# Kernel tuning notes

Hardware: AMD Instinct MI355X
Metric: run time of the kernel (lower is better)

The kernel has to match this reference:

```python
import jax, jax.numpy as jnp
import numpy as np

# Block-sparse linear config: W is (OUT_F, IN_F) in BSR form with BS x BS blocks,
OUT_F, IN_F, BS, K = 4096, 4096, 64, 32
NROW, NCOL = OUT_F // BS, IN_F // BS   # 64, 64
NNZB = NROW * K                         # 2048 nonzero blocks
BATCH = 8192


def setup_inputs() -> dict:
    key = jax.random.key(0)
    k1, k2, k3 = jax.random.split(key, 3)
    x = jax.random.normal(k1, (BATCH, IN_F), jnp.float32)
    values = jax.random.normal(k2, (NNZB, BS, BS), jnp.float32) * 0.02
    bias = jax.random.normal(k3, (OUT_F,), jnp.float32) * 0.01
    # BSR structure: K sorted, distinct column-block indices per block-row.
    cols = np.stack([np.sort((r + 2 * np.arange(K)) % NCOL) for r in range(NROW)])
    col_indices = jnp.asarray(cols.reshape(-1), jnp.int32)          # [NNZB]
    crow_indices = jnp.arange(NROW + 1, dtype=jnp.int32) * K        # [NROW+1]
    return {"x": x, "values": values, "bias": bias,
            "crow_indices": crow_indices, "col_indices": col_indices}


def reference(x, values, bias, crow_indices, col_indices):
    # Expand BSR row pointers to per-block row ids (structure is static/int).
    counts = jnp.diff(crow_indices)
    row_ids = jnp.repeat(jnp.arange(NROW), counts, total_repeat_length=NNZB)
    # Scatter nonzero blocks into a dense weight (only ~67 MB, cheap vs the GEMM).
    Wb = jnp.zeros((NROW, NCOL, BS, BS), values.dtype).at[row_ids, col_indices].set(values)
    W = Wb.transpose(0, 2, 1, 3).reshape(OUT_F, IN_F)  # [out_features, in_features]
    # forward: (W @ x.T).T + bias  ==  x @ W.T + bias
    return x @ W.T + bias
```

## Files before the change

kernel.cpp:

```cpp
#include <hip/hip_runtime.h>
#include <stdint.h>


#define BATCH   8192
#define IN_F    4096
#define OUT_F   4096
#define BS      64
#define NROW    64
#define NNZB    2048
#define BM      256
#define LDS_A_BYTES 32768
#define LDS_B_BYTES 16384
#define BUF_BYTES   (LDS_A_BYTES + LDS_B_BYTES)
#define NBUF    2

typedef float f32x4 __attribute__((ext_vector_type(4)));
typedef short s16x8 __attribute__((ext_vector_type(8)));

__device__ __forceinline__ void async_copy16(const void* g, void* l) {
  __builtin_amdgcn_global_load_lds(
      (__attribute__((address_space(1))) void*)g,
      (__attribute__((address_space(3))) void*)l, 16, 0, 0);
}

__device__ __forceinline__ unsigned short f32_to_bf16(float f) {
  union { float f; uint32_t u; } v; v.f = f;
  return (unsigned short)((v.u + 0x7FFFu + ((v.u >> 16) & 1u)) >> 16);
}

__global__ void cvt_kernel(const float4* __restrict__ xin,
                           const float4* __restrict__ win,
                           ushort4* __restrict__ xout,
                           ushort4* __restrict__ wout, int nx4, int ntot4) {
  int i = blockIdx.x * blockDim.x + threadIdx.x;
  if (i >= ntot4) return;
  const float4* src; ushort4* dst; int j;
  if (i < nx4) { src = xin; dst = xout; j = i; }
  else         { src = win; dst = wout; j = i - nx4; }
  float4 v = src[j];
  ushort4 o;
  o.x = f32_to_bf16(v.x); o.y = f32_to_bf16(v.y);
  o.z = f32_to_bf16(v.z); o.w = f32_to_bf16(v.w);
  dst[j] = o;
}

__global__ __launch_bounds__(512) void bsr_gemm_pair_kernel(
    const unsigned short* __restrict__ xb,
    const unsigned short* __restrict__ wb,
    const float* __restrict__ bias,
    const int* __restrict__ crow,
    const int* __restrict__ cols,
    float* __restrict__ out) {
  __shared__ alignas(16) char smem[NBUF * BUF_BYTES];

  const int tid = threadIdx.x;
  const int w   = tid >> 6;
  const int l   = tid & 63;
  const int wm  = w & 3;
  const int wn  = w >> 2;
  const int p   = blockIdx.x;
  const int rA  = ((p >> 1) << 2) + (p & 1);
  const int rB  = rA + 2;
  const int m0  = blockIdx.y * BM;

  const int startA = crow[rA], endA = crow[rA + 1];
  const int startB = crow[rB], endB = crow[rB + 1];

  const int lr = l & 15;
  const int q  = l >> 4;

  int cvA = (startA + l < endA) ? cols[startA + l] : 0;
  int cvB = (startB + l < endB) ? cols[startB + l] : 0;

  int myc = 0, mypk = 0;
  int nt = 0;
  {
    int ia = startA, ib = startB;
    const int clA = (endA > startA) ? endA - 1 : 0;
    const int clB = (endB > startB) ? endB - 1 : 0;
    while ((ia < endA) || (ib < endB)) {
      const int ca = (ia < endA) ? __shfl(cvA, ia - startA) : 0x7fffffff;
      const int cb = (ib < endB) ? __shfl(cvB, ib - startB) : 0x7fffffff;
      const int c  = min(ca, cb);
      const int hA = (ca == c);
      const int hB = (cb == c);
      const int sA = hA ? ia : clA;
      const int sB = hB ? ib : clB;
      if (nt == l) { myc = c; mypk = sA | (sB << 12) | (hA << 24) | (hB << 25); }
      ia += hA; ib += hB; ++nt;
    }
  }

  f32x4 acc[4][4];
#pragma unroll
  for (int mi = 0; mi < 4; ++mi)
#pragma unroll
    for (int ni = 0; ni < 4; ++ni) {
      f32x4 z = {0.f, 0.f, 0.f, 0.f};
      acc[mi][ni] = z;
    }

  const int srow = tid >> 3;
  const int sswz = ((tid & 7) ^ (srow & 7)) << 3;
  const unsigned short* agbase =
      xb + (size_t)(m0 + srow) * IN_F + sswz;
  const int bgoff = (srow << 6) + sswz;

  auto stage = [&](int t, int buf) {
    const int c  = __shfl(myc, t);
    const int pk = __shfl(mypk, t);
    const int sA = pk & 0xfff;
    const int sB = (pk >> 12) & 0xfff;
    char* const al = smem + buf * BUF_BYTES + tid * 16;
    char* const bl = smem + buf * BUF_BYTES + LDS_A_BYTES + tid * 16;
    const unsigned short* ag = agbase + (size_t)c * BS;
#pragma unroll
    for (int it = 0; it < 4; ++it)
      async_copy16(ag + (size_t)(it * 64) * IN_F, al + it * 8192);
    async_copy16(wb + ((size_t)sA << 12) + bgoff, bl);
    async_copy16(wb + ((size_t)sB << 12) + bgoff, bl + 8192);
  };

  if (nt > 0) stage(0, 0);
  __syncthreads();
  int cur = 0;
  for (int t = 0; t < nt; ++t) {
    if (t + 1 < nt) stage(t + 1, cur ^ 1);

    const int pk = __shfl(mypk, t);
    const char* const cbase = smem + cur * BUF_BYTES;
    if ((pk >> (24 + wn)) & 1) {
      __builtin_amdgcn_s_setprio(1);
#pragma unroll
      for (int ks = 0; ks < 2; ++ks) {
        const int chunk = (((ks << 2) + q) ^ (l & 7)) << 4;
        s16x8 af[4], bf[4];
#pragma unroll
        for (int mi = 0; mi < 4; ++mi)
          af[mi] = *(const s16x8*)(cbase +
                     ((wm << 6) + (mi << 4) + lr) * 128 + chunk);
#pragma unroll
        for (int ni = 0; ni < 4; ++ni)
          bf[ni] = *(const s16x8*)(cbase + LDS_A_BYTES + (wn << 13) +
                     ((ni << 4) + lr) * 128 + chunk);
#pragma unroll
        for (int mi = 0; mi < 4; ++mi)
#pragma unroll
          for (int ni = 0; ni < 4; ++ni)
            acc[mi][ni] = __builtin_amdgcn_mfma_f32_16x16x32_bf16(
                af[mi], bf[ni], acc[mi][ni], 0, 0, 0);
      }
      __builtin_amdgcn_s_setprio(0);
    }
    __syncthreads();
    cur ^= 1;
  }

  const int rW = wn ? rB : rA;
  const int colg = (rW << 6) + lr;
#pragma unroll
  for (int ni = 0; ni < 4; ++ni) {
    const float bv = bias[colg + (ni << 4)];
#pragma unroll
    for (int mi = 0; mi < 4; ++mi) {
      float* op = out +
          (size_t)(m0 + (wm << 6) + (mi << 4) + (q << 2)) * OUT_F +
          colg + (ni << 4);
#pragma unroll
      for (int e = 0; e < 4; ++e)
        op[(size_t)e * OUT_F] = acc[mi][ni][e] + bv;
    }
  }
}

__global__ void fallback_kernel(const float* __restrict__ x,
                                const float* __restrict__ vals,
                                const float* __restrict__ bias,
                                const int* __restrict__ crow,
                                const int* __restrict__ cols,
                                float* __restrict__ out) {
  int idx = blockIdx.x * 256 + threadIdx.x;
  int m = idx >> 12;
  int n = idx & 4095;
  int r = n >> 6, nl = n & 63;
  float s = 0.f;
  int e = crow[r + 1];
  for (int i = crow[r]; i < e; ++i) {
    const float* xp = x + (size_t)m * IN_F + cols[i] * 64;
    const float* wp = vals + ((size_t)i << 12) + nl * 64;
    for (int k = 0; k < 64; ++k) s += xp[k] * wp[k];
  }
  out[idx] = s + bias[n];
}

extern "C" void kernel_launch(void* const* d_in, const int* in_sizes, int n_in,
                              void* d_out, int out_size, void* d_ws,
                              size_t ws_size, hipStream_t stream) {
  const float* x    = (const float*)d_in[0];
  const float* vals = (const float*)d_in[1];
  const float* bias = (const float*)d_in[2];
  const int*   crow = (const int*)d_in[3];
  const int*   cols = (const int*)d_in[4];
  float* out = (float*)d_out;

  const size_t x_elems = (size_t)BATCH * IN_F;
  const size_t w_elems = (size_t)NNZB * BS * BS;
  const size_t need = (x_elems + w_elems) * 2;

  if (ws_size >= need) {
    unsigned short* xb = (unsigned short*)d_ws;
    unsigned short* wbp = xb + x_elems;
    const int nx4 = (int)(x_elems / 4);
    const int ntot4 = (int)((x_elems + w_elems) / 4);
    cvt_kernel<<<(ntot4 + 255) / 256, 256, 0, stream>>>(
        (const float4*)x, (const float4*)vals,
        (ushort4*)xb, (ushort4*)wbp, nx4, ntot4);
    dim3 grid(NROW / 2, BATCH / BM);
    bsr_gemm_pair_kernel<<<grid, 512, 0, stream>>>(xb, wbp, bias, crow, cols,
                                                   out);
  } else {
    fallback_kernel<<<(BATCH * OUT_F) / 256, 256, 0, stream>>>(
        x, vals, bias, crow, cols, out);
  }
}
```

Measured before the change: 418.5 us.

## Halve block to 256 threads with single LDS buffer and two blocks per CU

Shrinks the workgroup from 8 to 4 waves, so each wave computes a 128x64 tile (8x4 MFMA accumulators instead of 4x4). Double buffering is replaced by a single 48 KB LDS buffer, with barriers before and after each stage, and launch bounds request two blocks per CU. The aim is to get overlap from having several resident blocks rather than from in-block prefetch, and to raise MFMA work per LDS fragment load. The cost is that load latency is now exposed inside each block, and the larger accumulator set raises register pressure.

Measured after the change: 378.0 us. 1.11x faster.

```diff
diff --git a/kernel.cpp b/kernel.cpp
--- a/kernel.cpp
+++ b/kernel.cpp
@@ -9,10 +9,8 @@
 #define NROW    64
 #define NNZB    2048
 #define BM      256
-#define LDS_A_BYTES 32768
-#define LDS_B_BYTES 16384
-#define BUF_BYTES   (LDS_A_BYTES + LDS_B_BYTES)
-#define NBUF    2
+#define LDS_A_BYTES (BM * BS * 2)
+#define LDS_B_BYTES (2 * BS * BS * 2)
 
 typedef float f32x4 __attribute__((ext_vector_type(4)));
 typedef short s16x8 __attribute__((ext_vector_type(8)));
@@ -44,20 +42,20 @@
   dst[j] = o;
 }
 
-__global__ __launch_bounds__(512) void bsr_gemm_pair_kernel(
+__global__ __launch_bounds__(256, 2) void bsr_gemm_pair_kernel(
     const unsigned short* __restrict__ xb,
     const unsigned short* __restrict__ wb,
     const float* __restrict__ bias,
     const int* __restrict__ crow,
     const int* __restrict__ cols,
     float* __restrict__ out) {
-  __shared__ alignas(16) char smem[NBUF * BUF_BYTES];
+  __shared__ alignas(16) char smem[LDS_A_BYTES + LDS_B_BYTES];
 
   const int tid = threadIdx.x;
   const int w   = tid >> 6;
   const int l   = tid & 63;
-  const int wm  = w & 3;
-  const int wn  = w >> 2;
+  const int wm  = w & 1;
+  const int wn  = w >> 1;
   const int p   = blockIdx.x;
   const int rA  = ((p >> 1) << 2) + (p & 1);
   const int rB  = rA + 2;
@@ -91,9 +89,9 @@
     }
   }
 
-  f32x4 acc[4][4];
-#pragma unroll
-  for (int mi = 0; mi < 4; ++mi)
+  f32x4 acc[8][4];
+#pragma unroll
+  for (int mi = 0; mi < 8; ++mi)
 #pragma unroll
     for (int ni = 0; ni < 4; ++ni) {
       f32x4 z = {0.f, 0.f, 0.f, 0.f};
@@ -105,46 +103,48 @@
   const unsigned short* agbase =
       xb + (size_t)(m0 + srow) * IN_F + sswz;
   const int bgoff = (srow << 6) + sswz;
-
-  auto stage = [&](int t, int buf) {
+  char* const alds = smem + tid * 16;
+  char* const blds = smem + LDS_A_BYTES + tid * 16;
+
+  auto stage = [&](int t) {
+    const int pk = __shfl(mypk, t);
     const int c  = __shfl(myc, t);
-    const int pk = __shfl(mypk, t);
     const int sA = pk & 0xfff;
     const int sB = (pk >> 12) & 0xfff;
-    char* const al = smem + buf * BUF_BYTES + tid * 16;
-    char* const bl = smem + buf * BUF_BYTES + LDS_A_BYTES + tid * 16;
     const unsigned short* ag = agbase + (size_t)c * BS;
 #pragma unroll
-    for (int it = 0; it < 4; ++it)
-      async_copy16(ag + (size_t)(it * 64) * IN_F, al + it * 8192);
-    async_copy16(wb + ((size_t)sA << 12) + bgoff, bl);
-    async_copy16(wb + ((size_t)sB << 12) + bgoff, bl + 8192);
+    for (int it = 0; it < 8; ++it)
+      async_copy16(ag + (size_t)(it * 32) * IN_F, alds + it * 4096);
+    const unsigned short* w0 = wb + ((size_t)sA << 12) + bgoff;
+    async_copy16(w0, blds);
+    async_copy16(w0 + 2048, blds + 4096);
+    const unsigned short* w1 = wb + ((size_t)sB << 12) + bgoff;
+    async_copy16(w1, blds + 8192);
+    async_copy16(w1 + 2048, blds + 12288);
   };
 
-  if (nt > 0) stage(0, 0);
-  __syncthreads();
-  int cur = 0;
   for (int t = 0; t < nt; ++t) {
-    if (t + 1 < nt) stage(t + 1, cur ^ 1);
+    __syncthreads();
+    stage(t);
+    __syncthreads();
 
     const int pk = __shfl(mypk, t);
-    const char* const cbase = smem + cur * BUF_BYTES;
     if ((pk >> (24 + wn)) & 1) {
       __builtin_amdgcn_s_setprio(1);
 #pragma unroll
       for (int ks = 0; ks < 2; ++ks) {
         const int chunk = (((ks << 2) + q) ^ (l & 7)) << 4;
-        s16x8 af[4], bf[4];
-#pragma unroll
-        for (int mi = 0; mi < 4; ++mi)
-          af[mi] = *(const s16x8*)(cbase +
-                     ((wm << 6) + (mi << 4) + lr) * 128 + chunk);
+        s16x8 af[8], bf[4];
+#pragma unroll
+        for (int mi = 0; mi < 8; ++mi)
+          af[mi] = *(const s16x8*)(smem +
+                     ((wm << 7) + (mi << 4) + lr) * 128 + chunk);
 #pragma unroll
         for (int ni = 0; ni < 4; ++ni)
-          bf[ni] = *(const s16x8*)(cbase + LDS_A_BYTES + (wn << 13) +
+          bf[ni] = *(const s16x8*)(smem + LDS_A_BYTES + (wn << 13) +
                      ((ni << 4) + lr) * 128 + chunk);
 #pragma unroll
-        for (int mi = 0; mi < 4; ++mi)
+        for (int mi = 0; mi < 8; ++mi)
 #pragma unroll
           for (int ni = 0; ni < 4; ++ni)
             acc[mi][ni] = __builtin_amdgcn_mfma_f32_16x16x32_bf16(
@@ -152,8 +152,6 @@
       }
       __builtin_amdgcn_s_setprio(0);
     }
-    __syncthreads();
-    cur ^= 1;
   }
 
   const int rW = wn ? rB : rA;
@@ -162,9 +160,9 @@
   for (int ni = 0; ni < 4; ++ni) {
     const float bv = bias[colg + (ni << 4)];
 #pragma unroll
-    for (int mi = 0; mi < 4; ++mi) {
+    for (int mi = 0; mi < 8; ++mi) {
       float* op = out +
-          (size_t)(m0 + (wm << 6) + (mi << 4) + (q << 2)) * OUT_F +
+          (size_t)(m0 + (wm << 7) + (mi << 4) + (q << 2)) * OUT_F +
           colg + (ni << 4);
 #pragma unroll
       for (int e = 0; e < 4; ++e)
@@ -216,7 +214,7 @@
         (const float4*)x, (const float4*)vals,
         (ushort4*)xb, (ushort4*)wbp, nx4, ntot4);
     dim3 grid(NROW / 2, BATCH / BM);
-    bsr_gemm_pair_kernel<<<grid, 512, 0, stream>>>(xb, wbp, bias, crow, cols,
+    bsr_gemm_pair_kernel<<<grid, 256, 0, stream>>>(xb, wbp, bias, crow, cols,
                                                    out);
   } else {
     fallback_kernel<<<(BATCH * OUT_F) / 256, 256, 0, stream>>>(
```
